# Kernel tuning notes

Measured on AMD Instinct MI355X. Metric: run time of the kernel, lower is better.

The kernel has to match this reference:

```python
import jax, jax.numpy as jnp
import numpy as np

N_ELECTRODES = 19
N_EDGES = N_ELECTRODES * N_ELECTRODES  # 361 dense per-graph connectivity
B = 8192                                # number of graphs in the batch
C_IN = 64
C_OUT = 64


def setup_inputs() -> dict:
    key = jax.random.key(0)
    k_x, k_ew, k_wr, k_wo, k_b = jax.random.split(key, 5)
    n_nodes = B * N_ELECTRODES

    x = jax.random.normal(k_x, (n_nodes, C_IN), dtype=jnp.float32)

    # Per-graph dense 19x19 edge list, tiled with node offsets per graph.
    src = np.repeat(np.arange(N_ELECTRODES), N_ELECTRODES)  # [361] source j
    dst = np.tile(np.arange(N_ELECTRODES), N_ELECTRODES)    # [361] target i
    offs = (np.arange(B) * N_ELECTRODES)[:, None]           # [B,1]
    edge_index = np.stack([
        (src[None, :] + offs).ravel(),
        (dst[None, :] + offs).ravel(),
    ]).astype(np.int32)                                      # [2, B*361]

    # Learned params: edge weights (init zeros in torch; use randn for a
    # non-degenerate softplus), GraphConv lin_rel (with bias) and lin_root.
    edge_weights = 0.1 * jax.random.normal(k_ew, (N_EDGES,), dtype=jnp.float32)
    W_rel = jax.random.normal(k_wr, (C_OUT, C_IN), dtype=jnp.float32) / np.sqrt(C_IN)
    W_root = jax.random.normal(k_wo, (C_OUT, C_IN), dtype=jnp.float32) / np.sqrt(C_IN)
    bias = 0.01 * jax.random.normal(k_b, (C_OUT,), dtype=jnp.float32)

    return {
        "x": x,
        "edge_weights": edge_weights,
        "W_rel": W_rel,
        "W_root": W_root,
        "bias": bias,
        "edge_index": jnp.asarray(edge_index),
    }


def reference(x, edge_weights, W_rel, W_root, bias, edge_index):
    # w = softplus(edge_weights), repeated once per graph in the batch
    w = jax.nn.softplus(edge_weights)                      # [361]
    n_graphs = edge_index.shape[1] // edge_weights.shape[0]
    w_exp = jnp.tile(w, n_graphs)                          # [E]

    src, dst = edge_index[0], edge_index[1]
    # GraphConv (PyG): out = lin_rel(sum_j w_ij * x_j) + lin_root(x_i)
    msg = x[src] * w_exp[:, None]                          # gather + scale [E, C_in]
    agg = jax.ops.segment_sum(msg, dst, num_segments=x.shape[0])  # scatter-add [N, C_in]
    return agg @ W_rel.T + x @ W_root.T + bias
```

## Files before the change

kernel.cpp:

```cpp
#include <hip/hip_runtime.h>

#define NE 19
#define CIN 64
#define Z1T_STRIDE 80
#define SLICE 5120
#define WS_AFRAG 16384

typedef float f32x4 __attribute__((ext_vector_type(4)));
typedef __bf16 bf16x4 __attribute__((ext_vector_type(4)));
typedef __bf16 bf16x8 __attribute__((ext_vector_type(8)));

__device__ __forceinline__ bf16x8 packW(const float* q) {
  f32x4 a = *(const f32x4*)q;
  f32x4 b = *(const f32x4*)(q + 4);
  bf16x8 h;
  h[0]=(__bf16)a[0]; h[1]=(__bf16)a[1]; h[2]=(__bf16)a[2]; h[3]=(__bf16)a[3];
  h[4]=(__bf16)b[0]; h[5]=(__bf16)b[1]; h[6]=(__bf16)b[2]; h[7]=(__bf16)b[3];
  return h;
}

__global__ void prep_kernel(const float* __restrict__ ew,
                            const float* __restrict__ Wrel,
                            const float* __restrict__ Wroot,
                            unsigned char* __restrict__ ws) {
  const int t = threadIdx.x, bid = blockIdx.x;
  if (bid < 4) {
    int fid = bid * 256 + t;
    int p = fid >> 9, kt = (fid >> 8) & 1, nt = (fid >> 6) & 3, lane = fid & 63;
    const float* Wsrc = p ? Wroot : Wrel;
    *(bf16x8*)(ws + fid * 16) =
        packW(Wsrc + (nt * 16 + (lane & 15)) * CIN + kt * 32 + (lane >> 4) * 8);
  } else if (t < 128) {
    int mt = t >> 6, lane = t & 63;
    int row = mt * 16 + (lane & 15);
    bf16x8 h;
    #pragma unroll
    for (int b = 0; b < 8; ++b) {
      int k = (lane >> 4) * 8 + b;
      float v = 0.0f;
      if (row < NE && k < NE) {
        float z = ew[k * NE + row];
        v = fmaxf(z, 0.0f) + log1pf(expf(-fabsf(z)));
      }
      h[b] = (__bf16)v;
    }
    *(bf16x8*)(ws + WS_AFRAG + t * 16) = h;
  }
}

__global__ __launch_bounds__(64, 2) void gconv_kernel(
    const float* __restrict__ x, const float* __restrict__ bias,
    const unsigned char* __restrict__ ws, float* __restrict__ out)
{
  __shared__ __align__(16) unsigned char sl[SLICE];

  const int lane = threadIdx.x & 63;
  const int g0 = blockIdx.x * 2;
  const int lr = lane & 15, hg = lane >> 4;
  const bf16x8* frB = (const bf16x8*)ws;

  auto LOADAF = [&](bf16x8 af[2][2], int g) {
    const float* xg = x + (long long)g * NE * CIN;
    #pragma unroll
    for (int mt = 0; mt < 2; ++mt) {
      int rr = mt * 16 + lr; if (rr > NE - 1) rr = NE - 1;
      const float* xr = xg + rr * CIN + hg * 8;
      #pragma unroll
      for (int kt = 0; kt < 2; ++kt) af[mt][kt] = packW(xr + kt * 32);
    }
  };
  bf16x8 afa[2][2], afb[2][2];
  LOADAF(afa, g0);
  LOADAF(afb, g0 + 1);

  bf16x8 bfa[8], bfb[8];
  #pragma unroll
  for (int i = 0; i < 8; ++i) bfa[i] = frB[i * 64 + lane];
  #pragma unroll
  for (int i = 0; i < 8; ++i) bfb[i] = frB[(8 + i) * 64 + lane];
  const bf16x8 afm0 = frB[1024 + lane];
  const bf16x8 afm1 = frB[1088 + lane];
  float biasv[4];
  #pragma unroll
  for (int nt = 0; nt < 4; ++nt) biasv[nt] = bias[nt * 16 + lr];

  auto PROC = [&](bf16x8 af[2][2], unsigned char* z1, int g) {
    f32x4 zacc[2][4];
    #pragma unroll
    for (int mt = 0; mt < 2; ++mt)
      #pragma unroll
      for (int nt = 0; nt < 4; ++nt) { zacc[mt][nt][0]=0.f; zacc[mt][nt][1]=0.f; zacc[mt][nt][2]=0.f; zacc[mt][nt][3]=0.f; }
    #pragma unroll
    for (int nt = 0; nt < 4; ++nt)
      #pragma unroll
      for (int mt = 0; mt < 2; ++mt) {
        zacc[mt][nt] = __builtin_amdgcn_mfma_f32_16x16x32_bf16(
            af[mt][0], bfa[nt], zacc[mt][nt], 0, 0, 0);
        zacc[mt][nt] = __builtin_amdgcn_mfma_f32_16x16x32_bf16(
            af[mt][1], bfa[4 + nt], zacc[mt][nt], 0, 0, 0);
      }
    #pragma unroll
    for (int nt = 0; nt < 4; ++nt) {
      int c = nt * 16 + lr;
      bf16x4 h0;
      #pragma unroll
      for (int b = 0; b < 4; ++b) h0[b] = (__bf16)zacc[0][nt][b];
      *(bf16x4*)(z1 + c * Z1T_STRIDE + hg * 8) = h0;
      bf16x4 h1;
      #pragma unroll
      for (int b = 0; b < 4; ++b) {
        int j = 16 + hg * 4 + b;
        h1[b] = (j < NE) ? (__bf16)zacc[1][nt][b] : (__bf16)0.0f;
      }
      *(bf16x4*)(z1 + c * Z1T_STRIDE + 32 + hg * 8) = h1;
    }

    f32x4 acc[2][4];
    #pragma unroll
    for (int mt = 0; mt < 2; ++mt)
      #pragma unroll
      for (int nt = 0; nt < 4; ++nt) { acc[mt][nt][0]=0.f; acc[mt][nt][1]=0.f; acc[mt][nt][2]=0.f; acc[mt][nt][3]=0.f; }
    #pragma unroll
    for (int nt = 0; nt < 4; ++nt)
      #pragma unroll
      for (int mt = 0; mt < 2; ++mt) {
        acc[mt][nt] = __builtin_amdgcn_mfma_f32_16x16x32_bf16(
            af[mt][0], bfb[nt], acc[mt][nt], 0, 0, 0);
        acc[mt][nt] = __builtin_amdgcn_mfma_f32_16x16x32_bf16(
            af[mt][1], bfb[4 + nt], acc[mt][nt], 0, 0, 0);
      }
    #pragma unroll
    for (int nt = 0; nt < 4; ++nt) {
      bf16x8 zf = *(const bf16x8*)(z1 + (nt * 16 + lr) * Z1T_STRIDE + hg * 16);
      acc[0][nt] = __builtin_amdgcn_mfma_f32_16x16x32_bf16(afm0, zf, acc[0][nt], 0, 0, 0);
      acc[1][nt] = __builtin_amdgcn_mfma_f32_16x16x32_bf16(afm1, zf, acc[1][nt], 0, 0, 0);
    }
    float* og = out + (long long)g * NE * CIN;
    #pragma unroll
    for (int mt = 0; mt < 2; ++mt)
      #pragma unroll
      for (int nt = 0; nt < 4; ++nt)
        #pragma unroll
        for (int b = 0; b < 4; ++b) {
          int row = mt * 16 + hg * 4 + b;
          if (row < NE)
            og[row * CIN + nt * 16 + lr] = acc[mt][nt][b] + biasv[nt];
        }
  };

  PROC(afa, sl, g0);
  PROC(afb, sl, g0 + 1);
}

extern "C" void kernel_launch(void* const* d_in, const int* in_sizes, int n_in,
                              void* d_out, int out_size, void* d_ws, size_t ws_size,
                              hipStream_t stream) {
  const float* x    = (const float*)d_in[0];
  const float* ew   = (const float*)d_in[1];
  const float* Wrel = (const float*)d_in[2];
  const float* Wroot= (const float*)d_in[3];
  const float* bias = (const float*)d_in[4];
  float* out = (float*)d_out;
  unsigned char* ws = (unsigned char*)d_ws;

  prep_kernel<<<5, 256, 0, stream>>>(ew, Wrel, Wroot, ws);

  const int ngraphs = (in_sizes[0] / CIN) / NE;
  const int nblocks = ngraphs / 2;
  gconv_kernel<<<nblocks, 64, 0, stream>>>(x, bias, ws, out);
}
```

Measured before the change: 25.68 us.

## Fuse weight prep into main kernel with 4-wave blocks and prefetched graphs

New measurement: 24.21 us. 1.06x faster.

```diff
diff --git a/kernel.cpp b/kernel.cpp
--- a/kernel.cpp
+++ b/kernel.cpp
@@ -4,7 +4,8 @@
 #define CIN 64
 #define Z1T_STRIDE 80
 #define SLICE 5120
-#define WS_AFRAG 16384
+#define FRAG_BYTES 18432
+#define WAVES 4
 
 typedef float f32x4 __attribute__((ext_vector_type(4)));
 typedef __bf16 bf16x4 __attribute__((ext_vector_type(4)));
@@ -19,45 +20,20 @@
   return h;
 }
 
-__global__ void prep_kernel(const float* __restrict__ ew,
-                            const float* __restrict__ Wrel,
-                            const float* __restrict__ Wroot,
-                            unsigned char* __restrict__ ws) {
-  const int t = threadIdx.x, bid = blockIdx.x;
-  if (bid < 4) {
-    int fid = bid * 256 + t;
-    int p = fid >> 9, kt = (fid >> 8) & 1, nt = (fid >> 6) & 3, lane = fid & 63;
-    const float* Wsrc = p ? Wroot : Wrel;
-    *(bf16x8*)(ws + fid * 16) =
-        packW(Wsrc + (nt * 16 + (lane & 15)) * CIN + kt * 32 + (lane >> 4) * 8);
-  } else if (t < 128) {
-    int mt = t >> 6, lane = t & 63;
-    int row = mt * 16 + (lane & 15);
-    bf16x8 h;
-    #pragma unroll
-    for (int b = 0; b < 8; ++b) {
-      int k = (lane >> 4) * 8 + b;
-      float v = 0.0f;
-      if (row < NE && k < NE) {
-        float z = ew[k * NE + row];
-        v = fmaxf(z, 0.0f) + log1pf(expf(-fabsf(z)));
-      }
-      h[b] = (__bf16)v;
-    }
-    *(bf16x8*)(ws + WS_AFRAG + t * 16) = h;
-  }
-}
+__global__ __launch_bounds__(256, 2) void gconv_kernel(
+    const float* __restrict__ x, const float* __restrict__ ew,
+    const float* __restrict__ Wrel, const float* __restrict__ Wroot,
+    const float* __restrict__ bias, float* __restrict__ out)
+{
+  __shared__ __align__(16) unsigned char sl[FRAG_BYTES + WAVES * SLICE];
 
-__global__ __launch_bounds__(64, 2) void gconv_kernel(
-    const float* __restrict__ x, const float* __restrict__ bias,
-    const unsigned char* __restrict__ ws, float* __restrict__ out)
-{
-  __shared__ __align__(16) unsigned char sl[SLICE];
-
-  const int lane = threadIdx.x & 63;
-  const int g0 = blockIdx.x * 2;
+  const int t = threadIdx.x;
+  const int lane = t & 63;
+  const int wv = t >> 6;
+  const int g0 = blockIdx.x * (4 * WAVES) + wv * 4;
   const int lr = lane & 15, hg = lane >> 4;
-  const bf16x8* frB = (const bf16x8*)ws;
+  unsigned char* z1 = sl + FRAG_BYTES + wv * SLICE;
+  const bf16x8* frB = (const bf16x8*)sl;
 
   auto LOADAF = [&](bf16x8 af[2][2], int g) {
     const float* xg = x + (long long)g * NE * CIN;
@@ -73,6 +49,32 @@
   LOADAF(afa, g0);
   LOADAF(afb, g0 + 1);
 
+  #pragma unroll
+  for (int i = 0; i < 4; ++i) {
+    int fid = i * 256 + t;
+    int p = fid >> 9, kt = (fid >> 8) & 1, nt = (fid >> 6) & 3, fl = fid & 63;
+    const float* Wsrc = p ? Wroot : Wrel;
+    *(bf16x8*)(sl + fid * 16) =
+        packW(Wsrc + (nt * 16 + (fl & 15)) * CIN + kt * 32 + (fl >> 4) * 8);
+  }
+  if (t < 128) {
+    int mt = t >> 6, fl = t & 63;
+    int row = mt * 16 + (fl & 15);
+    bf16x8 h;
+    #pragma unroll
+    for (int b = 0; b < 8; ++b) {
+      int k = (fl >> 4) * 8 + b;
+      float v = 0.0f;
+      if (row < NE && k < NE) {
+        float z = ew[k * NE + row];
+        v = fmaxf(z, 0.0f) + log1pf(expf(-fabsf(z)));
+      }
+      h[b] = (__bf16)v;
+    }
+    *(bf16x8*)(sl + 16384 + t * 16) = h;
+  }
+  __syncthreads();
+
   bf16x8 bfa[8], bfb[8];
   #pragma unroll
   for (int i = 0; i < 8; ++i) bfa[i] = frB[i * 64 + lane];
@@ -84,7 +86,7 @@
   #pragma unroll
   for (int nt = 0; nt < 4; ++nt) biasv[nt] = bias[nt * 16 + lr];
 
-  auto PROC = [&](bf16x8 af[2][2], unsigned char* z1, int g) {
+  auto PROC = [&](bf16x8 af[2][2], int g) {
     f32x4 zacc[2][4];
     #pragma unroll
     for (int mt = 0; mt < 2; ++mt)
@@ -148,8 +150,12 @@
         }
   };
 
-  PROC(afa, sl, g0);
-  PROC(afb, sl, g0 + 1);
+  PROC(afa, g0);
+  LOADAF(afa, g0 + 2);
+  PROC(afb, g0 + 1);
+  LOADAF(afb, g0 + 3);
+  PROC(afa, g0 + 2);
+  PROC(afb, g0 + 3);
 }
 
 extern "C" void kernel_launch(void* const* d_in, const int* in_sizes, int n_in,
@@ -161,11 +167,8 @@
   const float* Wroot= (const float*)d_in[3];
   const float* bias = (const float*)d_in[4];
   float* out = (float*)d_out;
-  unsigned char* ws = (unsigned char*)d_ws;
-
-  prep_kernel<<<5, 256, 0, stream>>>(ew, Wrel, Wroot, ws);
 
   const int ngraphs = (in_sizes[0] / CIN) / NE;
-  const int nblocks = ngraphs / 2;
-  gconv_kernel<<<nblocks, 64, 0, stream>>>(x, bias, ws, out);
+  const int nblocks = ngraphs / 16;
+  gconv_kernel<<<nblocks, 256, 0, stream>>>(x, ew, Wrel, Wroot, bias, out);
 }
```
